# Kernel optimization log

Measured on AMD Instinct MI355X. Metric: run time of the kernel, lower is better.

The kernel has to match this reference:

```python
import jax, jax.numpy as jnp
import numpy as np

B, S, D = 2, 2048, 768
E, TOP_K = 8, 2
H = 4 * D  # expert hidden dim


def setup_inputs() -> dict:
    key = jax.random.key(0)
    ks = jax.random.split(key, 8)
    s_in = 1.0 / np.sqrt(D)
    s_h = 1.0 / np.sqrt(H)
    return {
        "x": jax.random.normal(ks[0], (B, S, D), dtype=jnp.float32),
        "gate_w": jax.random.uniform(ks[1], (D, E), jnp.float32, -s_in, s_in),
        "gate_b": jax.random.uniform(ks[2], (E,), jnp.float32, -s_in, s_in),
        "w1": jax.random.uniform(ks[3], (E, D, H), jnp.float32, -s_in, s_in),
        "b1": jax.random.uniform(ks[4], (E, H), jnp.float32, -s_in, s_in),
        "w2": jax.random.uniform(ks[5], (E, H, D), jnp.float32, -s_h, s_h),
        "b2": jax.random.uniform(ks[6], (E, D), jnp.float32, -s_h, s_h),
    }


def reference(x, gate_w, gate_b, w1, b1, w2, b2):
    # Router: gate linear -> top-k -> softmax over the k selected logits
    logits = jnp.einsum("bsd,de->bse", x, gate_w) + gate_b          # [B,S,E]
    top_vals, top_idx = jax.lax.top_k(logits, TOP_K)                 # [B,S,K]
    rw = jax.nn.softmax(top_vals, axis=-1)                           # [B,S,K]
    # Per-token per-expert combine weight (0 for unselected experts)
    onehot = jax.nn.one_hot(top_idx, E, dtype=x.dtype)               # [B,S,K,E]
    expert_w = jnp.einsum("bske,bsk->bse", onehot, rw)               # [B,S,E]

    # Expert MLPs (GELU exact, matching torch nn.GELU default; dropout is
    # identity in eval). Stacked as grouped GEMMs over the expert axis.
    h = jax.nn.gelu(jnp.einsum("bsd,edh->bseh", x, w1) + b1, approximate=False)
    y = jnp.einsum("bseh,ehd->bsed", h, w2) + b2                     # [B,S,E,D]
    # Weighted combine over experts
    return jnp.einsum("bse,bsed->bsd", expert_w, y)                  # [B,S,D]
```

## Files before the change

kernel.cpp:

```cpp
#include <hip/hip_runtime.h>
#include <hip/hip_bf16.h>

#define D_ 768
#define E_ 8
#define H_ 3072
#define N_TOK 4096
#define BT 64
#define BK 64

typedef _Float16 f16;
typedef f16 f16x8 __attribute__((ext_vector_type(8)));
typedef float f32x4 __attribute__((ext_vector_type(4)));

__device__ __forceinline__ void gld16(const f16* g, f16* l) {
    __builtin_amdgcn_global_load_lds(
        (const __attribute__((address_space(1))) unsigned int*)g,
        (__attribute__((address_space(3))) unsigned int*)l, 16, 0, 0);
}

__device__ __forceinline__ int prefix_off(const int* counts, int e, int* cnt_out) {
    int off = 0, cnt = 0;
#pragma unroll
    for (int q = 0; q < E_; q++) {
        int cq = counts[q];
        if (q < e) off += cq;
        if (q == e) cnt = cq;
    }
    *cnt_out = cnt;
    return off;
}

__global__ __launch_bounds__(256) void cvt_w_both(const float* __restrict__ w1,
                                                  const float* __restrict__ w2,
                                                  f16* __restrict__ w1t,
                                                  f16* __restrict__ w2t) {
    __shared__ f16 t[64][66];
    int z = blockIdx.z;
    const float* src; f16* dst; int R, C, xb, yb;
    int bx = blockIdx.x;
    if (z < E_) {
        src = w1 + (size_t)z * D_ * H_; dst = w1t + (size_t)z * D_ * H_;
        R = D_; C = H_; xb = bx % 48; yb = bx / 48;
    } else {
        src = w2 + (size_t)(z - E_) * H_ * D_; dst = w2t + (size_t)(z - E_) * H_ * D_;
        R = H_; C = D_; xb = bx % 12; yb = bx / 12;
    }
    int r0 = yb * 64, c0 = xb * 64;
    int tid = threadIdx.x;
    {
        int r = tid >> 4;
        int c = (tid & 15) * 4;
#pragma unroll
        for (int i = 0; i < 4; i++) {
            float4 v = *(const float4*)(src + (size_t)(r0 + r + i * 16) * C + (c0 + c));
            t[r + i * 16][c] = (f16)v.x;
            t[r + i * 16][c + 1] = (f16)v.y;
            t[r + i * 16][c + 2] = (f16)v.z;
            t[r + i * 16][c + 3] = (f16)v.w;
        }
    }
    __syncthreads();
    {
        int c = tid >> 3;
        int rr = (tid & 7) * 8;
        int ch = rr >> 3;
#pragma unroll
        for (int i = 0; i < 2; i++) {
            int cc = c + i * 32;
            int rowi = c0 + cc;
            f16x8 o;
#pragma unroll
            for (int j = 0; j < 8; j++) o[j] = t[rr + j][cc];
            *(f16x8*)(dst + (size_t)rowi * R + r0 + (((ch ^ rowi) & 7) << 3)) = o;
        }
    }
}

__global__ __launch_bounds__(1024) void router(const float* __restrict__ x,
                                               const float* __restrict__ gw,
                                               const float* __restrict__ gb,
                                               int* __restrict__ counts,
                                               int* __restrict__ list,
                                               float* __restrict__ wslot) {
    __shared__ int lcount[E_];
    __shared__ int lbase[E_];
    __shared__ int te0[64], te1[64], ts0[64], ts1[64];
    __shared__ float tw0[64], tw1[64];

    int tid = threadIdx.x;
    int wv = tid >> 6, lane = tid & 63;
    int s = lane >> 3, eL = lane & 7;
    if (tid < E_) lcount[tid] = 0;
    __syncthreads();

    float biasL = gb[eL];

#pragma unroll 1
    for (int i = 0; i < 4; i++) {
        int lt = wv * 4 + i;
        int tok = blockIdx.x * 64 + lt;
        const float* xr = x + (size_t)tok * D_;
        float a = 0.f;
        const float* gwl = gw + lane;
#pragma unroll 8
        for (int j = 0; j < 96; j++)
            a = fmaf(xr[j * 8 + s], gwl[j * 64], a);
        a += __shfl_xor(a, 8, 64);
        a += __shfl_xor(a, 16, 64);
        a += __shfl_xor(a, 32, 64);
        float lg = a + biasL;
        float le[8];
#pragma unroll
        for (int q = 0; q < 8; q++) le[q] = __shfl(lg, q, 64);
        float v0 = -3.4e38f, v1 = -3.4e38f;
        int i0 = 0, i1 = 0;
#pragma unroll
        for (int q = 0; q < 8; q++) {
            float l = le[q];
            if (l > v0) { v1 = v0; i1 = i0; v0 = l; i0 = q; }
            else if (l > v1) { v1 = l; i1 = q; }
        }
        if (lane == 0) {
            float p1 = expf(v1 - v0);
            float ssum = 1.f + p1;
            int s0 = atomicAdd(&lcount[i0], 1);
            int s1 = atomicAdd(&lcount[i1], 1);
            te0[lt] = i0; ts0[lt] = s0; tw0[lt] = 1.f / ssum;
            te1[lt] = i1; ts1[lt] = s1; tw1[lt] = p1 / ssum;
        }
    }
    __syncthreads();
    if (tid < E_) lbase[tid] = atomicAdd(&counts[tid], lcount[tid]);
    __syncthreads();
    if (tid < 64) {
        int tok = blockIdx.x * 64 + tid;
        int e0 = te0[tid], e1 = te1[tid];
        list[e0 * N_TOK + lbase[e0] + ts0[tid]] = tok * 2;
        list[e1 * N_TOK + lbase[e1] + ts1[tid]] = tok * 2 + 1;
        wslot[tok * 2] = tw0[tid];
        wslot[tok * 2 + 1] = tw1[tid];
    }
}

__global__ __launch_bounds__(256) void pack_a(const float* __restrict__ x,
                                              const int* __restrict__ counts,
                                              const int* __restrict__ list,
                                              f16* __restrict__ xg) {
    int wv = threadIdx.x >> 6, lane = threadIdx.x & 63;
    int idx = blockIdx.x * 4 + wv;
    int e = idx >> 12, j = idx & (N_TOK - 1);
    int cnt;
    int off = prefix_off(counts, e, &cnt);
    if (j >= cnt) return;
    int id = list[idx];
    int row = off + j;
    const float* xr = x + (size_t)(id >> 1) * D_;
    f16* dst = xg + (size_t)row * D_;
    int r7 = row & 7;
#pragma unroll
    for (int c = 0; c < 3; c++) {
        int h = lane * 4 + c * 256;
        float4 v = *(const float4*)(xr + h);
        f16 o[4] = {(f16)v.x, (f16)v.y, (f16)v.z, (f16)v.w};
        int hs = (h & ~0x3F) | ((((h >> 3) ^ r7) & 7) << 3) | (h & 7);
        *(float2*)(dst + hs) = *(const float2*)o;
    }
}

__global__ __launch_bounds__(256, 8) void gemm1(const f16* __restrict__ xg,
                                                const f16* __restrict__ w1t,
                                                const float* __restrict__ b1,
                                                const int* __restrict__ counts,
                                                f16* __restrict__ hbuf) {
    int bid = blockIdx.x;
    int e = bid & 7;
    int r = bid >> 3;
    int xb24 = r % 24;
    int yb = (r / 24) % 64;
    int xh = r / (24 * 64);
    int cnt;
    int off = prefix_off(counts, e, &cnt);
    int rb = yb * BT;
    if (rb >= cnt) return;
    int cb = (xh * 24 + xb24) * BT;

    __shared__ f16 lds[2 * BT * BK];
    char* ldsb = (char*)lds;

    int tid = threadIdx.x;
    int wv = tid >> 6, lane = tid & 63;
    int lr = lane >> 3, lc = lane & 7;

    int r0l = wv * 8 + lr;
    int r1l = 32 + wv * 8 + lr;
    int ag0 = off + rb + r0l; if (ag0 > 8191) ag0 = 8191;
    int ag1 = off + rb + r1l; if (ag1 > 8191) ag1 = 8191;
    const f16* ap0 = xg + (size_t)ag0 * D_ + lc * 8;
    const f16* ap1 = xg + (size_t)ag1 * D_ + lc * 8;
    const f16* wb = w1t + (size_t)e * H_ * D_;
    const f16* bp0 = wb + (size_t)(cb + r0l) * D_ + lc * 8;
    const f16* bp1 = wb + (size_t)(cb + r1l) * D_ + lc * 8;
    f16* la0 = lds + wv * 512;
    f16* la1 = lds + 2048 + wv * 512;
    f16* lb0 = lds + 4096 + wv * 512;
    f16* lb1 = lds + 6144 + wv * 512;

    int wr = (wv >> 1) * 32, wc = (wv & 1) * 32;
    int fr = lane & 15, qh = lane >> 4;
    int koff = (off + rb) & 7;

    int roA[2][2], roB[2][2];
#pragma unroll
    for (int m = 0; m < 2; m++)
#pragma unroll
        for (int ks = 0; ks < 2; ks++) {
            int row = wr + m * 16 + fr;
            roA[m][ks] = row * 128 + ((((ks * 4 + qh) ^ (koff + row)) & 7) << 4);
            int rwb = wc + m * 16 + fr;
            roB[m][ks] = 8192 + rwb * 128 + ((((ks * 4 + qh) ^ rwb) & 7) << 4);
        }

    f32x4 acc[2][2] = {};
    const int NT = D_ / BK;
#pragma unroll 1
    for (int t = 0; t < NT; ++t) {
        int kk = t * BK;
        gld16(ap0 + kk, la0);
        gld16(ap1 + kk, la1);
        gld16(bp0 + kk, lb0);
        gld16(bp1 + kk, lb1);
        __syncthreads();
#pragma unroll
        for (int ks = 0; ks < 2; ks++) {
            f16x8 a0 = *(const f16x8*)(ldsb + roA[0][ks]);
            f16x8 a1 = *(const f16x8*)(ldsb + roA[1][ks]);
            f16x8 b0 = *(const f16x8*)(ldsb + roB[0][ks]);
            f16x8 b1v = *(const f16x8*)(ldsb + roB[1][ks]);
            acc[0][0] = __builtin_amdgcn_mfma_f32_16x16x32_f16(a0, b0, acc[0][0], 0, 0, 0);
            acc[0][1] = __builtin_amdgcn_mfma_f32_16x16x32_f16(a0, b1v, acc[0][1], 0, 0, 0);
            acc[1][0] = __builtin_amdgcn_mfma_f32_16x16x32_f16(a1, b0, acc[1][0], 0, 0, 0);
            acc[1][1] = __builtin_amdgcn_mfma_f32_16x16x32_f16(a1, b1v, acc[1][1], 0, 0, 0);
        }
        __syncthreads();
    }

#pragma unroll
    for (int n = 0; n < 2; n++) {
        int colg = cb + wc + n * 16 + fr;
        float bias = b1[e * H_ + colg];
#pragma unroll
        for (int m = 0; m < 2; m++) {
#pragma unroll
            for (int r2 = 0; r2 < 4; r2++) {
                int j = rb + wr + m * 16 + qh * 4 + r2;
                if (j < cnt) {
                    float v = acc[m][n][r2] + bias;
                    v = 0.5f * v * (1.f + erff(v * 0.70710678f));
                    int row = off + j;
                    int hs = (colg & ~0x3F) | ((((colg >> 3) ^ row) & 7) << 3) | (colg & 7);
                    hbuf[(size_t)row * H_ + hs] = (f16)v;
                }
            }
        }
    }
}

#define KSPLIT 2
#define KCH (H_ / KSPLIT)
__global__ __launch_bounds__(256, 8) void gemm2(const f16* __restrict__ hbuf,
                                                const f16* __restrict__ w2t,
                                                const float* __restrict__ b2,
                                                const int* __restrict__ counts,
                                                const int* __restrict__ list,
                                                const float* __restrict__ wslot,
                                                float* __restrict__ out) {
    int bid = blockIdx.x;
    int e = bid & 7;
    int r = bid >> 3;
    int cb12 = r % 12;
    int yb = (r / 12) % 64;
    int kz = r / (12 * 64);
    int cnt;
    int off = prefix_off(counts, e, &cnt);
    int rb = yb * BT;
    if (rb >= cnt) return;
    int cb = cb12 * BT;
    int k0 = kz * KCH;

    __shared__ f16 lds[2 * BT * BK];
    char* ldsb = (char*)lds;

    int tid = threadIdx.x;
    int wv = tid >> 6, lane = tid & 63;
    int lr = lane >> 3, lc = lane & 7;

    int r0l = wv * 8 + lr;
    int r1l = 32 + wv * 8 + lr;
    int ag0 = off + rb + r0l; if (ag0 > 8191) ag0 = 8191;
    int ag1 = off + rb + r1l; if (ag1 > 8191) ag1 = 8191;
    const f16* ap0 = hbuf + (size_t)ag0 * H_ + k0 + lc * 8;
    const f16* ap1 = hbuf + (size_t)ag1 * H_ + k0 + lc * 8;
    const f16* wb = w2t + (size_t)e * D_ * H_;
    const f16* bp0 = wb + (size_t)(cb + r0l) * H_ + k0 + lc * 8;
    const f16* bp1 = wb + (size_t)(cb + r1l) * H_ + k0 + lc * 8;
    f16* la0 = lds + wv * 512;
    f16* la1 = lds + 2048 + wv * 512;
    f16* lb0 = lds + 4096 + wv * 512;
    f16* lb1 = lds + 6144 + wv * 512;

    int wr = (wv >> 1) * 32, wc = (wv & 1) * 32;
    int fr = lane & 15, qh = lane >> 4;
    int koff = (off + rb) & 7;

    int roA[2][2], roB[2][2];
#pragma unroll
    for (int m = 0; m < 2; m++)
#pragma unroll
        for (int ks = 0; ks < 2; ks++) {
            int row = wr + m * 16 + fr;
            roA[m][ks] = row * 128 + ((((ks * 4 + qh) ^ (koff + row)) & 7) << 4);
            int rwb = wc + m * 16 + fr;
            roB[m][ks] = 8192 + rwb * 128 + ((((ks * 4 + qh) ^ rwb) & 7) << 4);
        }

    f32x4 acc[2][2] = {};
    const int NT = KCH / BK;
#pragma unroll 1
    for (int t = 0; t < NT; ++t) {
        int kk = t * BK;
        gld16(ap0 + kk, la0);
        gld16(ap1 + kk, la1);
        gld16(bp0 + kk, lb0);
        gld16(bp1 + kk, lb1);
        __syncthreads();
#pragma unroll
        for (int ks = 0; ks < 2; ks++) {
            f16x8 a0 = *(const f16x8*)(ldsb + roA[0][ks]);
            f16x8 a1 = *(const f16x8*)(ldsb + roA[1][ks]);
            f16x8 b0 = *(const f16x8*)(ldsb + roB[0][ks]);
            f16x8 b1v = *(const f16x8*)(ldsb + roB[1][ks]);
            acc[0][0] = __builtin_amdgcn_mfma_f32_16x16x32_f16(a0, b0, acc[0][0], 0, 0, 0);
            acc[0][1] = __builtin_amdgcn_mfma_f32_16x16x32_f16(a0, b1v, acc[0][1], 0, 0, 0);
            acc[1][0] = __builtin_amdgcn_mfma_f32_16x16x32_f16(a1, b0, acc[1][0], 0, 0, 0);
            acc[1][1] = __builtin_amdgcn_mfma_f32_16x16x32_f16(a1, b1v, acc[1][1], 0, 0, 0);
        }
        __syncthreads();
    }

#pragma unroll
    for (int n = 0; n < 2; n++) {
        int colg = cb + wc + n * 16 + fr;
        float bias = (kz == 0) ? b2[e * D_ + colg] : 0.f;
#pragma unroll
        for (int m = 0; m < 2; m++) {
#pragma unroll
            for (int r2 = 0; r2 < 4; r2++) {
                int j = rb + wr + m * 16 + qh * 4 + r2;
                if (j < cnt) {
                    int id = list[e * N_TOK + j];
                    float w = wslot[id];
                    float v = (acc[m][n][r2] + bias) * w;
                    atomicAdd(&out[(size_t)(id >> 1) * D_ + colg], v);
                }
            }
        }
    }
}

extern "C" void kernel_launch(void* const* d_in, const int* in_sizes, int n_in,
                              void* d_out, int out_size, void* d_ws, size_t ws_size,
                              hipStream_t stream) {
    const float* x = (const float*)d_in[0];
    const float* gate_w = (const float*)d_in[1];
    const float* gate_b = (const float*)d_in[2];
    const float* w1 = (const float*)d_in[3];
    const float* b1 = (const float*)d_in[4];
    const float* w2 = (const float*)d_in[5];
    const float* b2 = (const float*)d_in[6];
    float* out = (float*)d_out;

    char* ws = (char*)d_ws;
    int* counts = (int*)ws;
    int* list = (int*)(ws + 1024);
    float* wslot = (float*)(ws + 132096);
    f16* xg = (f16*)(ws + 196608);
    f16* w1t = (f16*)(ws + 12779520);
    f16* w2t = (f16*)(ws + 50528256);
    f16* hbuf = (f16*)(ws + 88276992);

    hipMemsetAsync(counts, 0, 256, stream);
    hipMemsetAsync(out, 0, (size_t)out_size * sizeof(float), stream);

    router<<<64, 1024, 0, stream>>>(x, gate_w, gate_b, counts, list, wslot);
    pack_a<<<E_ * N_TOK / 4, 256, 0, stream>>>(x, counts, list, xg);
    cvt_w_both<<<dim3(576, 1, 16), 256, 0, stream>>>(w1, w2, w1t, w2t);
    gemm1<<<E_ * 2 * 64 * 24, 256, 0, stream>>>(xg, w1t, b1, counts, hbuf);
    gemm2<<<E_ * 2 * 64 * 12, 256, 0, stream>>>(hbuf, w2t, b2, counts, list, wslot, out);
}
```

Measured before the change: 252.8 us.

## Enlarge GEMM tiles to 128x128 with BK=32 and new swizzle, raise K-split

Both expert GEMMs move from 64x64 tiles with BK=64 to 128x128 tiles with BK=32, so each wave computes a 64x64 sub-tile (4x4 MFMA accumulators) and reuses each fragment across more MFMAs. The LDS swizzle is redesigned for 64-byte rows and applied consistently in weight conversion, packing and hbuf writes. gemm2 K-split goes from 2 to 4 to keep enough blocks, which doubles the atomic adds into the output. Larger tiles reduce global and LDS traffic per FLOP but raise register pressure (launch bounds lowered to 5) and waste more work on partially filled row tiles per expert.

```diff
diff --git a/kernel.cpp b/kernel.cpp
--- a/kernel.cpp
+++ b/kernel.cpp
@@ -5,8 +5,9 @@
 #define E_ 8
 #define H_ 3072
 #define N_TOK 4096
-#define BT 64
-#define BK 64
+#define BM 128
+#define BN 128
+#define BK 32
 
 typedef _Float16 f16;
 typedef f16 f16x8 __attribute__((ext_vector_type(8)));
@@ -28,6 +29,12 @@
     }
     *cnt_out = cnt;
     return off;
+}
+
+__device__ __forceinline__ int swz_pos(int h, int row) {
+    int q = (h >> 3) & 3;
+    int p = (((q ^ (row & 3)) + ((row >> 2) & 3)) & 3);
+    return (h & ~0x1F) | (p << 3) | (h & 7);
 }
 
 __global__ __launch_bounds__(256) void cvt_w_both(const float* __restrict__ w1,
@@ -63,7 +70,6 @@
     {
         int c = tid >> 3;
         int rr = (tid & 7) * 8;
-        int ch = rr >> 3;
 #pragma unroll
         for (int i = 0; i < 2; i++) {
             int cc = c + i * 32;
@@ -71,7 +77,7 @@
             f16x8 o;
 #pragma unroll
             for (int j = 0; j < 8; j++) o[j] = t[rr + j][cc];
-            *(f16x8*)(dst + (size_t)rowi * R + r0 + (((ch ^ rowi) & 7) << 3)) = o;
+            *(f16x8*)(dst + (size_t)rowi * R + swz_pos(r0 + rr, rowi)) = o;
         }
     }
 }
@@ -156,18 +162,16 @@
     int row = off + j;
     const float* xr = x + (size_t)(id >> 1) * D_;
     f16* dst = xg + (size_t)row * D_;
-    int r7 = row & 7;
 #pragma unroll
     for (int c = 0; c < 3; c++) {
         int h = lane * 4 + c * 256;
         float4 v = *(const float4*)(xr + h);
         f16 o[4] = {(f16)v.x, (f16)v.y, (f16)v.z, (f16)v.w};
-        int hs = (h & ~0x3F) | ((((h >> 3) ^ r7) & 7) << 3) | (h & 7);
-        *(float2*)(dst + hs) = *(const float2*)o;
-    }
-}
-
-__global__ __launch_bounds__(256, 8) void gemm1(const f16* __restrict__ xg,
+        *(float2*)(dst + swz_pos(h, row)) = *(const float2*)o;
+    }
+}
+
+__global__ __launch_bounds__(256, 5) void gemm1(const f16* __restrict__ xg,
                                                 const f16* __restrict__ w1t,
                                                 const float* __restrict__ b1,
                                                 const int* __restrict__ counts,
@@ -175,52 +179,51 @@
     int bid = blockIdx.x;
     int e = bid & 7;
     int r = bid >> 3;
-    int xb24 = r % 24;
-    int yb = (r / 24) % 64;
-    int xh = r / (24 * 64);
+    int xb12 = r % 12;
+    int yb = (r / 12) % 32;
+    int xh = r / (12 * 32);
     int cnt;
     int off = prefix_off(counts, e, &cnt);
-    int rb = yb * BT;
+    int rb = yb * BM;
     if (rb >= cnt) return;
-    int cb = (xh * 24 + xb24) * BT;
-
-    __shared__ f16 lds[2 * BT * BK];
+    int cb = (xh * 12 + xb12) * BN;
+
+    __shared__ f16 lds[2 * BM * BK];
     char* ldsb = (char*)lds;
 
     int tid = threadIdx.x;
-    int wv = tid >> 6, lane = tid & 63;
-    int lr = lane >> 3, lc = lane & 7;
-
-    int r0l = wv * 8 + lr;
-    int r1l = 32 + wv * 8 + lr;
-    int ag0 = off + rb + r0l; if (ag0 > 8191) ag0 = 8191;
-    int ag1 = off + rb + r1l; if (ag1 > 8191) ag1 = 8191;
-    const f16* ap0 = xg + (size_t)ag0 * D_ + lc * 8;
-    const f16* ap1 = xg + (size_t)ag1 * D_ + lc * 8;
-    const f16* wb = w1t + (size_t)e * H_ * D_;
-    const f16* bp0 = wb + (size_t)(cb + r0l) * D_ + lc * 8;
-    const f16* bp1 = wb + (size_t)(cb + r1l) * D_ + lc * 8;
-    f16* la0 = lds + wv * 512;
-    f16* la1 = lds + 2048 + wv * 512;
-    f16* lb0 = lds + 4096 + wv * 512;
-    f16* lb1 = lds + 6144 + wv * 512;
-
-    int wr = (wv >> 1) * 32, wc = (wv & 1) * 32;
-    int fr = lane & 15, qh = lane >> 4;
-    int koff = (off + rb) & 7;
-
-    int roA[2][2], roB[2][2];
-#pragma unroll
-    for (int m = 0; m < 2; m++)
-#pragma unroll
-        for (int ks = 0; ks < 2; ks++) {
-            int row = wr + m * 16 + fr;
-            roA[m][ks] = row * 128 + ((((ks * 4 + qh) ^ (koff + row)) & 7) << 4);
-            int rwb = wc + m * 16 + fr;
-            roB[m][ks] = 8192 + rwb * 128 + ((((ks * 4 + qh) ^ rwb) & 7) << 4);
-        }
-
-    f32x4 acc[2][2] = {};
+    int w = tid >> 6, l = tid & 63;
+
+    int arow0 = w * 16 + (l >> 2);
+    int arow1 = 64 + arow0;
+    int ag0 = off + rb + arow0; if (ag0 > 8191) ag0 = 8191;
+    int ag1 = off + rb + arow1; if (ag1 > 8191) ag1 = 8191;
+    const f16* ap0 = xg + (size_t)ag0 * D_ + (l & 3) * 8;
+    const f16* ap1 = xg + (size_t)ag1 * D_ + (l & 3) * 8;
+    const f16* bbase = w1t + (size_t)e * H_ * D_;
+    const f16* bp0 = bbase + (size_t)(cb + arow0) * D_ + (l & 3) * 8;
+    const f16* bp1 = bbase + (size_t)(cb + arow1) * D_ + (l & 3) * 8;
+    f16* la0 = lds + w * 512;
+    f16* la1 = lds + 2048 + w * 512;
+    f16* lb0 = lds + 4096 + w * 512;
+    f16* lb1 = lds + 6144 + w * 512;
+
+    int wr = (w >> 1) * 64, wc = (w & 1) * 64;
+    int fr = l & 15, qh = l >> 4;
+
+    int roA[4], roB[4];
+#pragma unroll
+    for (int m = 0; m < 4; m++) {
+        int rA = wr + m * 16 + fr;
+        int g = off + rb + rA;
+        int pA = (((qh ^ (g & 3)) + ((g >> 2) & 3)) & 3);
+        roA[m] = rA * 64 + pA * 16;
+        int rB = wc + m * 16 + fr;
+        int pB = (((qh ^ (rB & 3)) + ((rB >> 2) & 3)) & 3);
+        roB[m] = 8192 + rB * 64 + pB * 16;
+    }
+
+    f32x4 acc[4][4] = {};
     const int NT = D_ / BK;
 #pragma unroll 1
     for (int t = 0; t < NT; ++t) {
@@ -230,26 +233,25 @@
         gld16(bp0 + kk, lb0);
         gld16(bp1 + kk, lb1);
         __syncthreads();
-#pragma unroll
-        for (int ks = 0; ks < 2; ks++) {
-            f16x8 a0 = *(const f16x8*)(ldsb + roA[0][ks]);
-            f16x8 a1 = *(const f16x8*)(ldsb + roA[1][ks]);
-            f16x8 b0 = *(const f16x8*)(ldsb + roB[0][ks]);
-            f16x8 b1v = *(const f16x8*)(ldsb + roB[1][ks]);
-            acc[0][0] = __builtin_amdgcn_mfma_f32_16x16x32_f16(a0, b0, acc[0][0], 0, 0, 0);
-            acc[0][1] = __builtin_amdgcn_mfma_f32_16x16x32_f16(a0, b1v, acc[0][1], 0, 0, 0);
-            acc[1][0] = __builtin_amdgcn_mfma_f32_16x16x32_f16(a1, b0, acc[1][0], 0, 0, 0);
-            acc[1][1] = __builtin_amdgcn_mfma_f32_16x16x32_f16(a1, b1v, acc[1][1], 0, 0, 0);
-        }
+        f16x8 af[4], bf[4];
+#pragma unroll
+        for (int m = 0; m < 4; m++) af[m] = *(const f16x8*)(ldsb + roA[m]);
+#pragma unroll
+        for (int n = 0; n < 4; n++) bf[n] = *(const f16x8*)(ldsb + roB[n]);
+#pragma unroll
+        for (int m = 0; m < 4; m++)
+#pragma unroll
+            for (int n = 0; n < 4; n++)
+                acc[m][n] = __builtin_amdgcn_mfma_f32_16x16x32_f16(af[m], bf[n], acc[m][n], 0, 0, 0);
         __syncthreads();
     }
 
 #pragma unroll
-    for (int n = 0; n < 2; n++) {
+    for (int n = 0; n < 4; n++) {
         int colg = cb + wc + n * 16 + fr;
         float bias = b1[e * H_ + colg];
 #pragma unroll
-        for (int m = 0; m < 2; m++) {
+        for (int m = 0; m < 4; m++) {
 #pragma unroll
             for (int r2 = 0; r2 < 4; r2++) {
                 int j = rb + wr + m * 16 + qh * 4 + r2;
@@ -257,17 +259,16 @@
                     float v = acc[m][n][r2] + bias;
                     v = 0.5f * v * (1.f + erff(v * 0.70710678f));
                     int row = off + j;
-                    int hs = (colg & ~0x3F) | ((((colg >> 3) ^ row) & 7) << 3) | (colg & 7);
-                    hbuf[(size_t)row * H_ + hs] = (f16)v;
+                    hbuf[(size_t)row * H_ + swz_pos(colg, row)] = (f16)v;
                 }
             }
         }
     }
 }
 
-#define KSPLIT 2
+#define KSPLIT 4
 #define KCH (H_ / KSPLIT)
-__global__ __launch_bounds__(256, 8) void gemm2(const f16* __restrict__ hbuf,
+__global__ __launch_bounds__(256, 5) void gemm2(const f16* __restrict__ hbuf,
                                                 const f16* __restrict__ w2t,
                                                 const float* __restrict__ b2,
                                                 const int* __restrict__ counts,
@@ -277,53 +278,52 @@
     int bid = blockIdx.x;
     int e = bid & 7;
     int r = bid >> 3;
-    int cb12 = r % 12;
-    int yb = (r / 12) % 64;
-    int kz = r / (12 * 64);
+    int cb6 = r % 6;
+    int yb = (r / 6) % 32;
+    int kz = r / (6 * 32);
     int cnt;
     int off = prefix_off(counts, e, &cnt);
-    int rb = yb * BT;
+    int rb = yb * BM;
     if (rb >= cnt) return;
-    int cb = cb12 * BT;
+    int cb = cb6 * BN;
     int k0 = kz * KCH;
 
-    __shared__ f16 lds[2 * BT * BK];
+    __shared__ f16 lds[2 * BM * BK];
     char* ldsb = (char*)lds;
 
     int tid = threadIdx.x;
-    int wv = tid >> 6, lane = tid & 63;
-    int lr = lane >> 3, lc = lane & 7;
-
-    int r0l = wv * 8 + lr;
-    int r1l = 32 + wv * 8 + lr;
-    int ag0 = off + rb + r0l; if (ag0 > 8191) ag0 = 8191;
-    int ag1 = off + rb + r1l; if (ag1 > 8191) ag1 = 8191;
-    const f16* ap0 = hbuf + (size_t)ag0 * H_ + k0 + lc * 8;
-    const f16* ap1 = hbuf + (size_t)ag1 * H_ + k0 + lc * 8;
-    const f16* wb = w2t + (size_t)e * D_ * H_;
-    const f16* bp0 = wb + (size_t)(cb + r0l) * H_ + k0 + lc * 8;
-    const f16* bp1 = wb + (size_t)(cb + r1l) * H_ + k0 + lc * 8;
-    f16* la0 = lds + wv * 512;
-    f16* la1 = lds + 2048 + wv * 512;
-    f16* lb0 = lds + 4096 + wv * 512;
-    f16* lb1 = lds + 6144 + wv * 512;
-
-    int wr = (wv >> 1) * 32, wc = (wv & 1) * 32;
-    int fr = lane & 15, qh = lane >> 4;
-    int koff = (off + rb) & 7;
-
-    int roA[2][2], roB[2][2];
-#pragma unroll
-    for (int m = 0; m < 2; m++)
-#pragma unroll
-        for (int ks = 0; ks < 2; ks++) {
-            int row = wr + m * 16 + fr;
-            roA[m][ks] = row * 128 + ((((ks * 4 + qh) ^ (koff + row)) & 7) << 4);
-            int rwb = wc + m * 16 + fr;
-            roB[m][ks] = 8192 + rwb * 128 + ((((ks * 4 + qh) ^ rwb) & 7) << 4);
-        }
-
-    f32x4 acc[2][2] = {};
+    int w = tid >> 6, l = tid & 63;
+
+    int arow0 = w * 16 + (l >> 2);
+    int arow1 = 64 + arow0;
+    int ag0 = off + rb + arow0; if (ag0 > 8191) ag0 = 8191;
+    int ag1 = off + rb + arow1; if (ag1 > 8191) ag1 = 8191;
+    const f16* ap0 = hbuf + (size_t)ag0 * H_ + k0 + (l & 3) * 8;
+    const f16* ap1 = hbuf + (size_t)ag1 * H_ + k0 + (l & 3) * 8;
+    const f16* bbase = w2t + (size_t)e * D_ * H_;
+    const f16* bp0 = bbase + (size_t)(cb + arow0) * H_ + k0 + (l & 3) * 8;
+    const f16* bp1 = bbase + (size_t)(cb + arow1) * H_ + k0 + (l & 3) * 8;
+    f16* la0 = lds + w * 512;
+    f16* la1 = lds + 2048 + w * 512;
+    f16* lb0 = lds + 4096 + w * 512;
+    f16* lb1 = lds + 6144 + w * 512;
+
+    int wr = (w >> 1) * 64, wc = (w & 1) * 64;
+    int fr = l & 15, qh = l >> 4;
+
+    int roA[4], roB[4];
+#pragma unroll
+    for (int m = 0; m < 4; m++) {
+        int rA = wr + m * 16 + fr;
+        int g = off + rb + rA;
+        int pA = (((qh ^ (g & 3)) + ((g >> 2) & 3)) & 3);
+        roA[m] = rA * 64 + pA * 16;
+        int rB = wc + m * 16 + fr;
+        int pB = (((qh ^ (rB & 3)) + ((rB >> 2) & 3)) & 3);
+        roB[m] = 8192 + rB * 64 + pB * 16;
+    }
+
+    f32x4 acc[4][4] = {};
     const int NT = KCH / BK;
 #pragma unroll 1
     for (int t = 0; t < NT; ++t) {
@@ -333,33 +333,32 @@
         gld16(bp0 + kk, lb0);
         gld16(bp1 + kk, lb1);
         __syncthreads();
-#pragma unroll
-        for (int ks = 0; ks < 2; ks++) {
-            f16x8 a0 = *(const f16x8*)(ldsb + roA[0][ks]);
-            f16x8 a1 = *(const f16x8*)(ldsb + roA[1][ks]);
-            f16x8 b0 = *(const f16x8*)(ldsb + roB[0][ks]);
-            f16x8 b1v = *(const f16x8*)(ldsb + roB[1][ks]);
-            acc[0][0] = __builtin_amdgcn_mfma_f32_16x16x32_f16(a0, b0, acc[0][0], 0, 0, 0);
-            acc[0][1] = __builtin_amdgcn_mfma_f32_16x16x32_f16(a0, b1v, acc[0][1], 0, 0, 0);
-            acc[1][0] = __builtin_amdgcn_mfma_f32_16x16x32_f16(a1, b0, acc[1][0], 0, 0, 0);
-            acc[1][1] = __builtin_amdgcn_mfma_f32_16x16x32_f16(a1, b1v, acc[1][1], 0, 0, 0);
-        }
+        f16x8 af[4], bf[4];
+#pragma unroll
+        for (int m = 0; m < 4; m++) af[m] = *(const f16x8*)(ldsb + roA[m]);
+#pragma unroll
+        for (int n = 0; n < 4; n++) bf[n] = *(const f16x8*)(ldsb + roB[n]);
+#pragma unroll
+        for (int m = 0; m < 4; m++)
+#pragma unroll
+            for (int n = 0; n < 4; n++)
+                acc[m][n] = __builtin_amdgcn_mfma_f32_16x16x32_f16(af[m], bf[n], acc[m][n], 0, 0, 0);
         __syncthreads();
     }
 
 #pragma unroll
-    for (int n = 0; n < 2; n++) {
+    for (int n = 0; n < 4; n++) {
         int colg = cb + wc + n * 16 + fr;
         float bias = (kz == 0) ? b2[e * D_ + colg] : 0.f;
 #pragma unroll
-        for (int m = 0; m < 2; m++) {
+        for (int m = 0; m < 4; m++) {
 #pragma unroll
             for (int r2 = 0; r2 < 4; r2++) {
                 int j = rb + wr + m * 16 + qh * 4 + r2;
                 if (j < cnt) {
                     int id = list[e * N_TOK + j];
-                    float w = wslot[id];
-                    float v = (acc[m][n][r2] + bias) * w;
+                    float wgt = wslot[id];
+                    float v = (acc[m][n][r2] + bias) * wgt;
                     atomicAdd(&out[(size_t)(id >> 1) * D_ + colg], v);
                 }
             }
@@ -394,6 +393,6 @@
     router<<<64, 1024, 0, stream>>>(x, gate_w, gate_b, counts, list, wslot);
     pack_a<<<E_ * N_TOK / 4, 256, 0, stream>>>(x, counts, list, xg);
     cvt_w_both<<<dim3(576, 1, 16), 256, 0, stream>>>(w1, w2, w1t, w2t);
-    gemm1<<<E_ * 2 * 64 * 24, 256, 0, stream>>>(xg, w1t, b1, counts, hbuf);
-    gemm2<<<E_ * 2 * 64 * 12, 256, 0, stream>>>(hbuf, w2t, b2, counts, list, wslot, out);
-}
+    gemm1<<<E_ * 2 * 32 * 12, 256, 0, stream>>>(xg, w1t, b1, counts, hbuf);
+    gemm2<<<E_ * KSPLIT * 32 * 6, 256, 0, stream>>>(hbuf, w2t, b2, counts, list, wslot, out);
+}
```

After: 351.5 us. 1.39x slower.

## Enlarge gemm2 tiles to 128x128 with double-buffered async LDS prefetch

Applied to the files above, without the earlier changes.

Rewrites the second expert GEMM to use 128x128 output tiles computed by 512-thread blocks, with each wave holding a 64x32 subtile. A two-stage LDS double buffer lets the next K-slice load while MFMAs run, gated by explicit vmcnt waits. The aim is more operand reuse per byte loaded and hiding global-load latency behind compute. The cost is larger LDS use (64KB) and more registers per thread, which lowers occupancy, and coarser tiles waste more work on partial expert row blocks.

```diff
diff --git a/kernel.cpp b/kernel.cpp
--- a/kernel.cpp
+++ b/kernel.cpp
@@ -267,7 +267,10 @@
 
 #define KSPLIT 2
 #define KCH (H_ / KSPLIT)
-__global__ __launch_bounds__(256, 8) void gemm2(const f16* __restrict__ hbuf,
+#define G2BM 128
+#define G2BN 128
+#define G2BK 64
+__global__ __launch_bounds__(512, 4) void gemm2(const f16* __restrict__ hbuf,
                                                 const f16* __restrict__ w2t,
                                                 const float* __restrict__ b2,
                                                 const int* __restrict__ counts,
@@ -277,89 +280,104 @@
     int bid = blockIdx.x;
     int e = bid & 7;
     int r = bid >> 3;
-    int cb12 = r % 12;
-    int yb = (r / 12) % 64;
-    int kz = r / (12 * 64);
+    int cb6 = r % 6;
+    int yb = (r / 6) % 32;
+    int kz = r / (6 * 32);
     int cnt;
     int off = prefix_off(counts, e, &cnt);
-    int rb = yb * BT;
+    int rb = yb * G2BM;
     if (rb >= cnt) return;
-    int cb = cb12 * BT;
+    int cb = cb6 * G2BN;
     int k0 = kz * KCH;
 
-    __shared__ f16 lds[2 * BT * BK];
+    __shared__ f16 lds[2 * (G2BM + G2BN) * G2BK];
     char* ldsb = (char*)lds;
 
     int tid = threadIdx.x;
-    int wv = tid >> 6, lane = tid & 63;
-    int lr = lane >> 3, lc = lane & 7;
-
-    int r0l = wv * 8 + lr;
-    int r1l = 32 + wv * 8 + lr;
-    int ag0 = off + rb + r0l; if (ag0 > 8191) ag0 = 8191;
-    int ag1 = off + rb + r1l; if (ag1 > 8191) ag1 = 8191;
-    const f16* ap0 = hbuf + (size_t)ag0 * H_ + k0 + lc * 8;
-    const f16* ap1 = hbuf + (size_t)ag1 * H_ + k0 + lc * 8;
-    const f16* wb = w2t + (size_t)e * D_ * H_;
-    const f16* bp0 = wb + (size_t)(cb + r0l) * H_ + k0 + lc * 8;
-    const f16* bp1 = wb + (size_t)(cb + r1l) * H_ + k0 + lc * 8;
-    f16* la0 = lds + wv * 512;
-    f16* la1 = lds + 2048 + wv * 512;
-    f16* lb0 = lds + 4096 + wv * 512;
-    f16* lb1 = lds + 6144 + wv * 512;
-
-    int wr = (wv >> 1) * 32, wc = (wv & 1) * 32;
-    int fr = lane & 15, qh = lane >> 4;
-    int koff = (off + rb) & 7;
-
-    int roA[2][2], roB[2][2];
-#pragma unroll
-    for (int m = 0; m < 2; m++)
+    int w = tid >> 6, l = tid & 63;
+    int fr = l & 15, qh = l >> 4;
+    int wm = w >> 2, wn = w & 3;
+
+    const f16* gpA[2]; const f16* gpB[2];
+    f16* lbA[2]; f16* lbB[2];
+#pragma unroll
+    for (int j = 0; j < 2; j++) {
+        int c = j * 512 + w * 64 + l;
+        int rowi = c >> 3, q = c & 7;
+        int ag = off + rb + rowi; if (ag > 8191) ag = 8191;
+        gpA[j] = hbuf + (size_t)ag * H_ + k0 + q * 8;
+        lbA[j] = lds + j * 4096 + w * 512;
+        gpB[j] = w2t + (size_t)e * D_ * H_ + (size_t)(cb + rowi) * H_ + k0 + q * 8;
+        lbB[j] = lds + 8192 + j * 4096 + w * 512;
+    }
+
+    int roA[4][2], roB[2][2];
+#pragma unroll
+    for (int m = 0; m < 4; m++)
 #pragma unroll
         for (int ks = 0; ks < 2; ks++) {
-            int row = wr + m * 16 + fr;
-            roA[m][ks] = row * 128 + ((((ks * 4 + qh) ^ (koff + row)) & 7) << 4);
-            int rwb = wc + m * 16 + fr;
-            roB[m][ks] = 8192 + rwb * 128 + ((((ks * 4 + qh) ^ rwb) & 7) << 4);
-        }
-
-    f32x4 acc[2][2] = {};
-    const int NT = KCH / BK;
+            int rA = wm * 64 + m * 16 + fr;
+            int g = off + rb + rA;
+            roA[m][ks] = rA * 128 + ((((ks * 4 + qh) ^ g) & 7) << 4);
+        }
+#pragma unroll
+    for (int n = 0; n < 2; n++)
+#pragma unroll
+        for (int ks = 0; ks < 2; ks++) {
+            int rB = wn * 32 + n * 16 + fr;
+            roB[n][ks] = 16384 + rB * 128 + ((((ks * 4 + qh) ^ rB) & 7) << 4);
+        }
+
+#define G2STAGE(t, buf) do {                                   \
+    int kko = (t) * G2BK;                                      \
+    gld16(gpA[0] + kko, lbA[0] + (buf) * 16384);               \
+    gld16(gpA[1] + kko, lbA[1] + (buf) * 16384);               \
+    gld16(gpB[0] + kko, lbB[0] + (buf) * 16384);               \
+    gld16(gpB[1] + kko, lbB[1] + (buf) * 16384);               \
+} while (0)
+
+    f32x4 acc[4][2] = {};
+    const int NT = KCH / G2BK;
+
+    G2STAGE(0, 0);
+    G2STAGE(1, 1);
+
 #pragma unroll 1
     for (int t = 0; t < NT; ++t) {
-        int kk = t * BK;
-        gld16(ap0 + kk, la0);
-        gld16(ap1 + kk, la1);
-        gld16(bp0 + kk, lb0);
-        gld16(bp1 + kk, lb1);
+        if (t + 1 < NT) asm volatile("s_waitcnt vmcnt(4)" ::: "memory");
+        else            asm volatile("s_waitcnt vmcnt(0)" ::: "memory");
         __syncthreads();
+        int bo = (t & 1) * 32768;
+        f16x8 af[4], bf[2];
 #pragma unroll
         for (int ks = 0; ks < 2; ks++) {
-            f16x8 a0 = *(const f16x8*)(ldsb + roA[0][ks]);
-            f16x8 a1 = *(const f16x8*)(ldsb + roA[1][ks]);
-            f16x8 b0 = *(const f16x8*)(ldsb + roB[0][ks]);
-            f16x8 b1v = *(const f16x8*)(ldsb + roB[1][ks]);
-            acc[0][0] = __builtin_amdgcn_mfma_f32_16x16x32_f16(a0, b0, acc[0][0], 0, 0, 0);
-            acc[0][1] = __builtin_amdgcn_mfma_f32_16x16x32_f16(a0, b1v, acc[0][1], 0, 0, 0);
-            acc[1][0] = __builtin_amdgcn_mfma_f32_16x16x32_f16(a1, b0, acc[1][0], 0, 0, 0);
-            acc[1][1] = __builtin_amdgcn_mfma_f32_16x16x32_f16(a1, b1v, acc[1][1], 0, 0, 0);
+#pragma unroll
+            for (int m = 0; m < 4; m++) af[m] = *(const f16x8*)(ldsb + bo + roA[m][ks]);
+#pragma unroll
+            for (int n = 0; n < 2; n++) bf[n] = *(const f16x8*)(ldsb + bo + roB[n][ks]);
+#pragma unroll
+            for (int m = 0; m < 4; m++)
+#pragma unroll
+                for (int n = 0; n < 2; n++)
+                    acc[m][n] = __builtin_amdgcn_mfma_f32_16x16x32_f16(af[m], bf[n], acc[m][n], 0, 0, 0);
         }
         __syncthreads();
+        if (t + 2 < NT) G2STAGE(t + 2, t & 1);
     }
 
 #pragma unroll
     for (int n = 0; n < 2; n++) {
-        int colg = cb + wc + n * 16 + fr;
+        int colg = cb + wn * 32 + n * 16 + fr;
         float bias = (kz == 0) ? b2[e * D_ + colg] : 0.f;
 #pragma unroll
-        for (int m = 0; m < 2; m++) {
+        for (int m = 0; m < 4; m++) {
 #pragma unroll
             for (int r2 = 0; r2 < 4; r2++) {
-                int j = rb + wr + m * 16 + qh * 4 + r2;
+                int j = rb + wm * 64 + m * 16 + qh * 4 + r2;
                 if (j < cnt) {
                     int id = list[e * N_TOK + j];
-                    float w = wslot[id];
-                    float v = (acc[m][n][r2] + bias) * w;
+                    float wgt = wslot[id];
+                    float v = (acc[m][n][r2] + bias) * wgt;
                     atomicAdd(&out[(size_t)(id >> 1) * D_ + colg], v);
                 }
             }
@@ -395,5 +413,5 @@
     pack_a<<<E_ * N_TOK / 4, 256, 0, stream>>>(x, counts, list, xg);
     cvt_w_both<<<dim3(576, 1, 16), 256, 0, stream>>>(w1, w2, w1t, w2t);
     gemm1<<<E_ * 2 * 64 * 24, 256, 0, stream>>>(xg, w1t, b1, counts, hbuf);
-    gemm2<<<E_ * 2 * 64 * 12, 256, 0, stream>>>(hbuf, w2t, b2, counts, list, wslot, out);
-}
+    gemm2<<<E_ * 2 * 32 * 6, 512, 0, stream>>>(hbuf, w2t, b2, counts, list, wslot, out);
+}
```

After: 270.8 us. 7.1% more time.

## Enlarge gemm1 tiles to 128x128 with 4x4 MFMA fragments per wave

Applied to the files above, without the earlier changes.

The first expert GEMM moves from 64x64 output tiles (2x2 MFMA fragments per wave) to 128x128 tiles with 4x4 fragments per wave. LDS grows to 32 KB, occupancy is lowered to 3 blocks per CU, and the grid shrinks to match. The aim is more data reuse per LDS load and fewer global loads per FLOP. The cost is more wasted rows on each expert's partial last tile, more register pressure, and fewer blocks available to hide latency.

```diff
diff --git a/kernel.cpp b/kernel.cpp
--- a/kernel.cpp
+++ b/kernel.cpp
@@ -167,7 +167,10 @@
     }
 }
 
-__global__ __launch_bounds__(256, 8) void gemm1(const f16* __restrict__ xg,
+#define G1BM 128
+#define G1BN 128
+#define G1BK 64
+__global__ __launch_bounds__(256, 3) void gemm1(const f16* __restrict__ xg,
                                                 const f16* __restrict__ w1t,
                                                 const float* __restrict__ b1,
                                                 const int* __restrict__ counts,
@@ -175,84 +178,84 @@
     int bid = blockIdx.x;
     int e = bid & 7;
     int r = bid >> 3;
-    int xb24 = r % 24;
-    int yb = (r / 24) % 64;
-    int xh = r / (24 * 64);
+    int xb12 = r % 12;
+    int yb = (r / 12) % 32;
+    int xh = r / (12 * 32);
     int cnt;
     int off = prefix_off(counts, e, &cnt);
-    int rb = yb * BT;
+    int rb = yb * G1BM;
     if (rb >= cnt) return;
-    int cb = (xh * 24 + xb24) * BT;
-
-    __shared__ f16 lds[2 * BT * BK];
+    int cb = (xh * 12 + xb12) * G1BN;
+
+    __shared__ f16 lds[(G1BM + G1BN) * G1BK];
     char* ldsb = (char*)lds;
 
     int tid = threadIdx.x;
-    int wv = tid >> 6, lane = tid & 63;
-    int lr = lane >> 3, lc = lane & 7;
-
-    int r0l = wv * 8 + lr;
-    int r1l = 32 + wv * 8 + lr;
-    int ag0 = off + rb + r0l; if (ag0 > 8191) ag0 = 8191;
-    int ag1 = off + rb + r1l; if (ag1 > 8191) ag1 = 8191;
-    const f16* ap0 = xg + (size_t)ag0 * D_ + lc * 8;
-    const f16* ap1 = xg + (size_t)ag1 * D_ + lc * 8;
-    const f16* wb = w1t + (size_t)e * H_ * D_;
-    const f16* bp0 = wb + (size_t)(cb + r0l) * D_ + lc * 8;
-    const f16* bp1 = wb + (size_t)(cb + r1l) * D_ + lc * 8;
-    f16* la0 = lds + wv * 512;
-    f16* la1 = lds + 2048 + wv * 512;
-    f16* lb0 = lds + 4096 + wv * 512;
-    f16* lb1 = lds + 6144 + wv * 512;
-
-    int wr = (wv >> 1) * 32, wc = (wv & 1) * 32;
-    int fr = lane & 15, qh = lane >> 4;
-    int koff = (off + rb) & 7;
-
-    int roA[2][2], roB[2][2];
-#pragma unroll
-    for (int m = 0; m < 2; m++)
+    int w = tid >> 6, l = tid & 63;
+    int fr = l & 15, qh = l >> 4;
+    int wm = w >> 1, wn = w & 1;
+
+    const f16* gpA[4]; const f16* gpB[4];
+    f16* lbA[4]; f16* lbB[4];
+#pragma unroll
+    for (int j = 0; j < 4; j++) {
+        int c = j * 256 + w * 64 + l;
+        int rowi = c >> 3, q = c & 7;
+        int ag = off + rb + rowi; if (ag > 8191) ag = 8191;
+        gpA[j] = xg + (size_t)ag * D_ + q * 8;
+        lbA[j] = lds + j * 2048 + w * 512;
+        gpB[j] = w1t + (size_t)e * H_ * D_ + (size_t)(cb + rowi) * D_ + q * 8;
+        lbB[j] = lds + 8192 + j * 2048 + w * 512;
+    }
+
+    int roA[4][2], roB[4][2];
+#pragma unroll
+    for (int m = 0; m < 4; m++)
 #pragma unroll
         for (int ks = 0; ks < 2; ks++) {
-            int row = wr + m * 16 + fr;
-            roA[m][ks] = row * 128 + ((((ks * 4 + qh) ^ (koff + row)) & 7) << 4);
-            int rwb = wc + m * 16 + fr;
-            roB[m][ks] = 8192 + rwb * 128 + ((((ks * 4 + qh) ^ rwb) & 7) << 4);
-        }
-
-    f32x4 acc[2][2] = {};
-    const int NT = D_ / BK;
+            int rA = wm * 64 + m * 16 + fr;
+            int g = off + rb + rA;
+            roA[m][ks] = rA * 128 + ((((ks * 4 + qh) ^ g) & 7) << 4);
+            int rB = wn * 64 + m * 16 + fr;
+            roB[m][ks] = 16384 + rB * 128 + ((((ks * 4 + qh) ^ rB) & 7) << 4);
+        }
+
+    f32x4 acc[4][4] = {};
+    const int NT = D_ / G1BK;
 #pragma unroll 1
     for (int t = 0; t < NT; ++t) {
-        int kk = t * BK;
-        gld16(ap0 + kk, la0);
-        gld16(ap1 + kk, la1);
-        gld16(bp0 + kk, lb0);
-        gld16(bp1 + kk, lb1);
+        int kk = t * G1BK;
+#pragma unroll
+        for (int j = 0; j < 4; j++) {
+            gld16(gpA[j] + kk, lbA[j]);
+            gld16(gpB[j] + kk, lbB[j]);
+        }
         __syncthreads();
 #pragma unroll
         for (int ks = 0; ks < 2; ks++) {
-            f16x8 a0 = *(const f16x8*)(ldsb + roA[0][ks]);
-            f16x8 a1 = *(const f16x8*)(ldsb + roA[1][ks]);
-            f16x8 b0 = *(const f16x8*)(ldsb + roB[0][ks]);
-            f16x8 b1v = *(const f16x8*)(ldsb + roB[1][ks]);
-            acc[0][0] = __builtin_amdgcn_mfma_f32_16x16x32_f16(a0, b0, acc[0][0], 0, 0, 0);
-            acc[0][1] = __builtin_amdgcn_mfma_f32_16x16x32_f16(a0, b1v, acc[0][1], 0, 0, 0);
-            acc[1][0] = __builtin_amdgcn_mfma_f32_16x16x32_f16(a1, b0, acc[1][0], 0, 0, 0);
-            acc[1][1] = __builtin_amdgcn_mfma_f32_16x16x32_f16(a1, b1v, acc[1][1], 0, 0, 0);
+            f16x8 af[4], bf[4];
+#pragma unroll
+            for (int m = 0; m < 4; m++) af[m] = *(const f16x8*)(ldsb + roA[m][ks]);
+#pragma unroll
+            for (int n = 0; n < 4; n++) bf[n] = *(const f16x8*)(ldsb + roB[n][ks]);
+#pragma unroll
+            for (int m = 0; m < 4; m++)
+#pragma unroll
+                for (int n = 0; n < 4; n++)
+                    acc[m][n] = __builtin_amdgcn_mfma_f32_16x16x32_f16(af[m], bf[n], acc[m][n], 0, 0, 0);
         }
         __syncthreads();
     }
 
 #pragma unroll
-    for (int n = 0; n < 2; n++) {
-        int colg = cb + wc + n * 16 + fr;
+    for (int n = 0; n < 4; n++) {
+        int colg = cb + wn * 64 + n * 16 + fr;
         float bias = b1[e * H_ + colg];
 #pragma unroll
-        for (int m = 0; m < 2; m++) {
+        for (int m = 0; m < 4; m++) {
 #pragma unroll
             for (int r2 = 0; r2 < 4; r2++) {
-                int j = rb + wr + m * 16 + qh * 4 + r2;
+                int j = rb + wm * 64 + m * 16 + qh * 4 + r2;
                 if (j < cnt) {
                     float v = acc[m][n][r2] + bias;
                     v = 0.5f * v * (1.f + erff(v * 0.70710678f));
@@ -394,6 +397,6 @@
     router<<<64, 1024, 0, stream>>>(x, gate_w, gate_b, counts, list, wslot);
     pack_a<<<E_ * N_TOK / 4, 256, 0, stream>>>(x, counts, list, xg);
     cvt_w_both<<<dim3(576, 1, 16), 256, 0, stream>>>(w1, w2, w1t, w2t);
-    gemm1<<<E_ * 2 * 64 * 24, 256, 0, stream>>>(xg, w1t, b1, counts, hbuf);
+    gemm1<<<E_ * 2 * 32 * 12, 256, 0, stream>>>(xg, w1t, b1, counts, hbuf);
     gemm2<<<E_ * 2 * 64 * 12, 256, 0, stream>>>(hbuf, w2t, b2, counts, list, wslot, out);
 }
```

Measured after the change: 256.3 us. Within noise of the previous version (+1.4%).
